# Kernel optimization log

Hardware: AMD Instinct MI355X
Metric: run time of the kernel (lower is better)

## Reference

```python
import jax, jax.numpy as jnp
import numpy as np
from math import sqrt

BASE = 10000.0  # rope_theta
NUM_HEADS = 16


def _quant(x):
    # per-row (last-dim) symmetric int8 fake-quant, matching ActivationQuantSTE.forward
    scale = 127.0 / jnp.maximum(jnp.max(jnp.abs(x), axis=-1, keepdims=True), 1e-5)
    return jnp.clip(jnp.round(x * scale), -128.0, 127.0) / scale


@jax.custom_vjp
def act_quant(x):
    return _quant(x)

def _aq_fwd(x):
    return _quant(x), None

def _aq_bwd(_, g):
    return (g,)  # straight-through estimator

act_quant.defvjp(_aq_fwd, _aq_bwd)


def complex_linear(xr, xi, Wr, Wi):
    # ComplexLinearBase: quantize activations, then
    #   y_real = q_real @ Wr^T + q_imag @ Wi^T
    #   y_imag = q_real @ Wi^T - q_imag @ Wr^T
    qr = act_quant(xr)
    qi = act_quant(xi)
    yr = qr @ Wr.T + qi @ Wi.T
    yi = qr @ Wi.T - qi @ Wr.T
    return yr, yi


def setup_inputs() -> dict:
    T, H = 2048, 2048
    key = jax.random.key(0)
    ks = jax.random.split(key, 10)
    w = lambda k: jax.random.normal(k, (H, H), jnp.float32) * 0.02
    return {
        "hidden_real": jax.random.normal(ks[0], (T, H), jnp.float32),
        "hidden_imag": jax.random.normal(ks[1], (T, H), jnp.float32),
        "positions": jnp.arange(T, dtype=jnp.int32),
        "Wq_r": w(ks[2]), "Wq_i": w(ks[3]),
        "Wk_r": w(ks[4]), "Wk_i": w(ks[5]),
        "Wv_r": w(ks[6]), "Wv_i": w(ks[7]),
        "Wo_r": w(ks[8]), "Wo_i": w(ks[9]),
    }


def reference(hidden_real, hidden_imag, positions, Wq_r, Wq_i, Wk_r, Wk_i, Wv_r, Wv_i, Wo_r, Wo_i):
    T, H = hidden_real.shape
    NH = NUM_HEADS
    D = H // NH  # head_dim

    # complex QKV projections with int8 activation fake-quant
    qr, qi = complex_linear(hidden_real, hidden_imag, Wq_r, Wq_i)
    kr, ki = complex_linear(hidden_real, hidden_imag, Wk_r, Wk_i)
    vr, vi = complex_linear(hidden_real, hidden_imag, Wv_r, Wv_i)

    # Complex RoPE: interleaving (real, imag) then GPT-J-style rotation with
    # head_size = rotary_dim = 2*D is equivalent to rotating (real, imag) pairs:
    #   out_real = real*cos - imag*sin ; out_imag = imag*cos + real*sin
    # inv_freq = base^-(arange(0, 2D, 2)/(2D)) = base^-(arange(D)/D), len D.
    inv_freq = 1.0 / (BASE ** (jnp.arange(D, dtype=jnp.float32) / D))
    freqs = positions.astype(jnp.float32)[:, None] * inv_freq[None, :]  # [T, D]
    # cache is stored in bf16 in the original module
    cos = jnp.cos(freqs).astype(jnp.bfloat16).astype(jnp.float32)[:, None, :]  # [T,1,D]
    sin = jnp.sin(freqs).astype(jnp.bfloat16).astype(jnp.float32)[:, None, :]

    def rope(xr_, xi_):
        r = xr_.reshape(T, NH, D)
        i = xi_.reshape(T, NH, D)
        return r * cos - i * sin, i * cos + r * sin

    qr3, qi3 = rope(qr, qi)
    kr3, ki3 = rope(kr, ki)
    vr3 = vr.reshape(T, NH, D)
    vi3 = vi.reshape(T, NH, D)

    # causal attention; scores = Re(q . conj(k)) / sqrt(2*D)  (complex dim is 2*D)
    scale = 1.0 / sqrt(2 * D)
    scores = (jnp.einsum('thd,shd->hts', qr3, kr3)
              + jnp.einsum('thd,shd->hts', qi3, ki3)) * scale  # [NH, T, T]
    causal = jnp.tril(jnp.ones((T, T), dtype=bool))
    scores = jnp.where(causal[None], scores, -1e9)
    p = jax.nn.softmax(scores, axis=-1)

    out_r = jnp.einsum('hts,shd->thd', p, vr3).reshape(T, H)
    out_i = jnp.einsum('hts,shd->thd', p, vi3).reshape(T, H)

    # complex output projection (with activation fake-quant)
    return complex_linear(out_r, out_i, Wo_r, Wo_i)
```

## Files before the change

### kernel.cpp

```cpp
#include <hip/hip_runtime.h>


typedef float v4f __attribute__((ext_vector_type(4)));
typedef _Float16 v8h __attribute__((ext_vector_type(8)));
typedef _Float16 v4h __attribute__((ext_vector_type(4)));

typedef const __attribute__((address_space(1))) void glob_void;
typedef __attribute__((address_space(3))) void lds_void;

__device__ __forceinline__ void gload16(const _Float16* gp, _Float16* lp) {
  __builtin_amdgcn_global_load_lds((glob_void*)gp, (lds_void*)lp, 16, 0, 0);
}

__device__ __forceinline__ float bf16_rt(float f) {
  union { float f; unsigned u; } a; a.f = f;
  unsigned r = (a.u + 0x7fffu + ((a.u >> 16) & 1u)) & 0xffff0000u;
  union { unsigned u; float f; } b; b.u = r;
  return b.f;
}

#define SBAR()  __builtin_amdgcn_sched_barrier(0)
#define WBAR()  __builtin_amdgcn_s_barrier()
#define LGKM0() asm volatile("s_waitcnt lgkmcnt(0)" ::: "memory")

__global__ __launch_bounds__(512, 2) void gemm_qkv256(
    const _Float16* __restrict__ A, const _Float16* __restrict__ B,
    _Float16* __restrict__ Yq, _Float16* __restrict__ vt)
{
  const int p = blockIdx.x;
  const int xcd = p & 7, s = p >> 3;
  const int mt = s & 7, ntl = s >> 3;
  const int nt = xcd * 8 + ntl;
  const int m0 = mt << 8;
  const int n0 = nt * 192;

  __shared__ __align__(16) _Float16 lds[57344];

  const int tid = threadIdx.x, lane = tid & 63, wave = tid >> 6;
  const int quad = lane >> 4, l15 = lane & 15;
  const int wm = wave >> 2, wn = wave & 3;

  const int rr = tid >> 2;
  const int lc8 = (((tid & 3) ^ ((tid >> 3) & 3)) << 3);
  const _Float16* gA = A + (long long)(m0 + rr) * 4096 + lc8;
  const _Float16* gBj[3];
#pragma unroll
  for (int j = 0; j < 3; ++j) {
    const int ks = (j == 2) || (j == 1 && tid >= 256);
    const int r = j * 128 + (tid >> 2) - ks * 192;
    gBj[j] = B + (long long)(n0 + r) * 4096 + ks * 32 + lc8;
  }

  const int co = ((quad ^ ((l15 >> 1) & 3)) << 3);
  const int aBase = (wm * 128 + l15) * 32 + co;
  const int bBase = (wn * 48 + l15) * 32 + co;

  v4f acc[8][3] = {};

  {
    _Float16* sd = lds + tid * 8;
    gload16(gA, sd);
    gload16(gA + 524288, sd + 4096);
    gload16(gBj[0], sd + 16384);
    gload16(gBj[1], sd + 20480);
    gload16(gA + 32, sd + 8192);
    gload16(gA + 524288 + 32, sd + 12288);
    gload16(gBj[2], sd + 24576);
  }
  asm volatile("s_waitcnt vmcnt(3)" ::: "memory");
  WBAR();

  for (int t = 0; t < 64; ++t) {
    const _Float16* As = lds + (t & 1) * 28672;
    const _Float16* Bs = As + 16384;
    _Float16* sd = lds + ((t & 1) ^ 1) * 28672 + tid * 8;
    const int k1 = (t + 1) << 6;
    const bool stg = (t < 63);

    v8h bf[3], af[4];

    af[0] = *(const v8h*)&As[aBase];
    af[1] = *(const v8h*)&As[aBase + 512];
    af[2] = *(const v8h*)&As[aBase + 1024];
    af[3] = *(const v8h*)&As[aBase + 1536];
    bf[0] = *(const v8h*)&Bs[bBase];
    bf[1] = *(const v8h*)&Bs[bBase + 512];
    bf[2] = *(const v8h*)&Bs[bBase + 1024];
    if (stg) { gload16(gA + k1, sd); gload16(gA + k1 + 524288, sd + 4096); }
    SBAR(); WBAR(); LGKM0(); SBAR();
    __builtin_amdgcn_s_setprio(1);
#pragma unroll
    for (int i = 0; i < 4; ++i)
#pragma unroll
      for (int nf = 0; nf < 3; ++nf)
        acc[i][nf] = __builtin_amdgcn_mfma_f32_16x16x32_f16(af[i], bf[nf], acc[i][nf], 0, 0, 0);
    __builtin_amdgcn_s_setprio(0);
    WBAR();

    af[0] = *(const v8h*)&As[aBase + 2048];
    af[1] = *(const v8h*)&As[aBase + 2560];
    af[2] = *(const v8h*)&As[aBase + 3072];
    af[3] = *(const v8h*)&As[aBase + 3584];
    if (stg) { gload16(gBj[0] + k1, sd + 16384); gload16(gBj[1] + k1, sd + 20480); }
    SBAR(); WBAR(); LGKM0(); SBAR();
    __builtin_amdgcn_s_setprio(1);
#pragma unroll
    for (int i = 0; i < 4; ++i)
#pragma unroll
      for (int nf = 0; nf < 3; ++nf)
        acc[4 + i][nf] = __builtin_amdgcn_mfma_f32_16x16x32_f16(af[i], bf[nf], acc[4 + i][nf], 0, 0, 0);
    __builtin_amdgcn_s_setprio(0);
    if (stg) asm volatile("s_waitcnt vmcnt(4)" ::: "memory");
    else     asm volatile("s_waitcnt vmcnt(0)" ::: "memory");
    WBAR();

    bf[0] = *(const v8h*)&Bs[bBase + 6144];
    bf[1] = *(const v8h*)&Bs[bBase + 6656];
    bf[2] = *(const v8h*)&Bs[bBase + 7168];
    af[0] = *(const v8h*)&As[aBase + 8192];
    af[1] = *(const v8h*)&As[aBase + 8704];
    af[2] = *(const v8h*)&As[aBase + 9216];
    af[3] = *(const v8h*)&As[aBase + 9728];
    if (stg) { gload16(gA + k1 + 32, sd + 8192); gload16(gA + k1 + 524288 + 32, sd + 12288); }
    SBAR(); WBAR(); LGKM0(); SBAR();
    __builtin_amdgcn_s_setprio(1);
#pragma unroll
    for (int i = 0; i < 4; ++i)
#pragma unroll
      for (int nf = 0; nf < 3; ++nf)
        acc[i][nf] = __builtin_amdgcn_mfma_f32_16x16x32_f16(af[i], bf[nf], acc[i][nf], 0, 0, 0);
    __builtin_amdgcn_s_setprio(0);
    WBAR();

    af[0] = *(const v8h*)&As[aBase + 10240];
    af[1] = *(const v8h*)&As[aBase + 10752];
    af[2] = *(const v8h*)&As[aBase + 11264];
    af[3] = *(const v8h*)&As[aBase + 11776];
    if (stg) gload16(gBj[2] + k1, sd + 24576);
    SBAR(); WBAR(); LGKM0(); SBAR();
    __builtin_amdgcn_s_setprio(1);
#pragma unroll
    for (int i = 0; i < 4; ++i)
#pragma unroll
      for (int nf = 0; nf < 3; ++nf)
        acc[4 + i][nf] = __builtin_amdgcn_mfma_f32_16x16x32_f16(af[i], bf[nf], acc[4 + i][nf], 0, 0, 0);
    __builtin_amdgcn_s_setprio(0);
    if (stg) asm volatile("s_waitcnt vmcnt(3)" ::: "memory");
    WBAR();
  }

#pragma unroll
  for (int mf = 0; mf < 8; ++mf) {
#pragma unroll
    for (int nf = 0; nf < 3; ++nf) {
      const int col = n0 + wn * 48 + nf * 16 + l15;
      const int row0 = m0 + wm * 128 + mf * 16 + quad * 4;
      if (col >= 8192) {
        const int c = col - 8192;
        const int hh = (c & 2047) >> 7;
        const int dcol = (c < 2048) ? (c & 127) : (128 + (c & 127));
        v4h pk;
#pragma unroll
        for (int r = 0; r < 4; ++r) pk[r] = (_Float16)acc[mf][nf][r];
        *(v4h*)(vt + ((long long)(hh * 256 + dcol)) * 2048 + row0) = pk;
      } else {
#pragma unroll
        for (int r = 0; r < 4; ++r)
          Yq[(long long)(row0 + r) * 8192 + col] = (_Float16)acc[mf][nf][r];
      }
    }
  }
}

__global__ __launch_bounds__(512, 2) void gemm_out256(
    const _Float16* __restrict__ A, const _Float16* __restrict__ B,
    float* __restrict__ O)
{
  const int p = blockIdx.x;
  const int xcd = p & 7, s = p >> 3;
  const int mt = s & 7, ntl = s >> 3;
  const int nt = xcd * 4 + ntl;
  const int m0 = mt << 8, n0 = nt << 7;

  __shared__ __align__(16) _Float16 lds[49152];

  const int tid = threadIdx.x, lane = tid & 63, wave = tid >> 6;
  const int quad = lane >> 4, l15 = lane & 15;
  const int wm = wave >> 2, wn = wave & 3;

  const int rr = tid >> 2;
  const int lc8 = (((tid & 3) ^ ((tid >> 3) & 3)) << 3);
  const _Float16* gA = A + (long long)(m0 + rr) * 4096 + lc8;
  const _Float16* gB = B + (long long)(n0 + rr) * 4096 + lc8;

  const int co = ((quad ^ ((l15 >> 1) & 3)) << 3);
  const int aBase = (wm * 128 + l15) * 32 + co;
  const int bBase = (wn * 32 + l15) * 32 + co;

  v4f acc[8][2] = {};

  {
    _Float16* sd = lds + tid * 8;
    gload16(gA, sd);
    gload16(gA + 524288, sd + 4096);
    gload16(gB, sd + 16384);
    gload16(gA + 32, sd + 8192);
    gload16(gA + 524288 + 32, sd + 12288);
    gload16(gB + 32, sd + 20480);
  }
  asm volatile("s_waitcnt vmcnt(3)" ::: "memory");
  WBAR();

  for (int t = 0; t < 64; ++t) {
    const _Float16* As = lds + (t & 1) * 24576;
    const _Float16* Bs = As + 16384;
    _Float16* sd = lds + ((t & 1) ^ 1) * 24576 + tid * 8;
    const int k1 = (t + 1) << 6;
    const bool stg = (t < 63);

    v8h bf[2], af[4];

    af[0] = *(const v8h*)&As[aBase];
    af[1] = *(const v8h*)&As[aBase + 512];
    af[2] = *(const v8h*)&As[aBase + 1024];
    af[3] = *(const v8h*)&As[aBase + 1536];
    bf[0] = *(const v8h*)&Bs[bBase];
    bf[1] = *(const v8h*)&Bs[bBase + 512];
    if (stg) { gload16(gA + k1, sd); gload16(gA + k1 + 524288, sd + 4096); }
    SBAR(); WBAR(); LGKM0(); SBAR();
    __builtin_amdgcn_s_setprio(1);
#pragma unroll
    for (int i = 0; i < 4; ++i)
#pragma unroll
      for (int nf = 0; nf < 2; ++nf)
        acc[i][nf] = __builtin_amdgcn_mfma_f32_16x16x32_f16(af[i], bf[nf], acc[i][nf], 0, 0, 0);
    __builtin_amdgcn_s_setprio(0);
    WBAR();

    af[0] = *(const v8h*)&As[aBase + 2048];
    af[1] = *(const v8h*)&As[aBase + 2560];
    af[2] = *(const v8h*)&As[aBase + 3072];
    af[3] = *(const v8h*)&As[aBase + 3584];
    if (stg) gload16(gB + k1, sd + 16384);
    SBAR(); WBAR(); LGKM0(); SBAR();
    __builtin_amdgcn_s_setprio(1);
#pragma unroll
    for (int i = 0; i < 4; ++i)
#pragma unroll
      for (int nf = 0; nf < 2; ++nf)
        acc[4 + i][nf] = __builtin_amdgcn_mfma_f32_16x16x32_f16(af[i], bf[nf], acc[4 + i][nf], 0, 0, 0);
    __builtin_amdgcn_s_setprio(0);
    if (stg) asm volatile("s_waitcnt vmcnt(3)" ::: "memory");
    else     asm volatile("s_waitcnt vmcnt(0)" ::: "memory");
    WBAR();

    bf[0] = *(const v8h*)&Bs[bBase + 4096];
    bf[1] = *(const v8h*)&Bs[bBase + 4608];
    af[0] = *(const v8h*)&As[aBase + 8192];
    af[1] = *(const v8h*)&As[aBase + 8704];
    af[2] = *(const v8h*)&As[aBase + 9216];
    af[3] = *(const v8h*)&As[aBase + 9728];
    if (stg) { gload16(gA + k1 + 32, sd + 8192); gload16(gA + k1 + 524288 + 32, sd + 12288); }
    SBAR(); WBAR(); LGKM0(); SBAR();
    __builtin_amdgcn_s_setprio(1);
#pragma unroll
    for (int i = 0; i < 4; ++i)
#pragma unroll
      for (int nf = 0; nf < 2; ++nf)
        acc[i][nf] = __builtin_amdgcn_mfma_f32_16x16x32_f16(af[i], bf[nf], acc[i][nf], 0, 0, 0);
    __builtin_amdgcn_s_setprio(0);
    WBAR();

    af[0] = *(const v8h*)&As[aBase + 10240];
    af[1] = *(const v8h*)&As[aBase + 10752];
    af[2] = *(const v8h*)&As[aBase + 11264];
    af[3] = *(const v8h*)&As[aBase + 11776];
    if (stg) gload16(gB + k1 + 32, sd + 20480);
    SBAR(); WBAR(); LGKM0(); SBAR();
    __builtin_amdgcn_s_setprio(1);
#pragma unroll
    for (int i = 0; i < 4; ++i)
#pragma unroll
      for (int nf = 0; nf < 2; ++nf)
        acc[4 + i][nf] = __builtin_amdgcn_mfma_f32_16x16x32_f16(af[i], bf[nf], acc[4 + i][nf], 0, 0, 0);
    __builtin_amdgcn_s_setprio(0);
    if (stg) asm volatile("s_waitcnt vmcnt(3)" ::: "memory");
    WBAR();
  }

#pragma unroll
  for (int mf = 0; mf < 8; ++mf) {
#pragma unroll
    for (int nf = 0; nf < 2; ++nf) {
      const int col = n0 + wn * 32 + nf * 16 + l15;
      const int row0 = m0 + wm * 128 + mf * 16 + quad * 4;
#pragma unroll
      for (int r = 0; r < 4; ++r) {
        const int row = row0 + r;
        const float v = acc[mf][nf][r];
        if (col < 2048) O[(long long)row * 2048 + col] = v;
        else O[2048ll * 2048 + (long long)row * 2048 + (col - 2048)] = v;
      }
    }
  }
}

__global__ __launch_bounds__(256) void quant_rows(
    const float* __restrict__ s0, const float* __restrict__ s1,
    _Float16* __restrict__ dst)
{
  const int t = blockIdx.x, y = blockIdx.y;
  const float* src = (y ? s1 : s0) + (long long)t * 2048;
  const int tid = threadIdx.x, lane = tid & 63, wave = tid >> 6;
  __shared__ float rbuf[4];
  const v4f a = *(const v4f*)(src + tid * 4);
  const v4f b = *(const v4f*)(src + 1024 + tid * 4);
  float m = 0.f;
#pragma unroll
  for (int k = 0; k < 4; ++k)
    m = fmaxf(m, fmaxf(fabsf(a[k]), fabsf(b[k])));
  for (int o = 1; o < 64; o <<= 1) m = fmaxf(m, __shfl_xor(m, o, 64));
  if (lane == 0) rbuf[wave] = m;
  __syncthreads();
  m = fmaxf(fmaxf(rbuf[0], rbuf[1]), fmaxf(rbuf[2], rbuf[3]));
  const float scale = 127.f / fmaxf(m, 1e-5f);
  const float inv = 1.f / scale;
  _Float16* d = dst + (long long)t * 4096 + (long long)y * 2048 + tid * 4;
  v4h qa, qb;
#pragma unroll
  for (int k = 0; k < 4; ++k) {
    qa[k] = (_Float16)(fminf(fmaxf(rintf(a[k] * scale), -128.f), 127.f) * inv);
    qb[k] = (_Float16)(fminf(fmaxf(rintf(b[k] * scale), -128.f), 127.f) * inv);
  }
  *(v4h*)d = qa;
  *(v4h*)(d + 1024) = qb;
}

__global__ __launch_bounds__(256) void wprep(
    const float* __restrict__ Wq_r, const float* __restrict__ Wq_i,
    const float* __restrict__ Wk_r, const float* __restrict__ Wk_i,
    const float* __restrict__ Wv_r, const float* __restrict__ Wv_i,
    const float* __restrict__ Wo_r, const float* __restrict__ Wo_i,
    _Float16* __restrict__ Bqkv, _Float16* __restrict__ Bo)
{
  const float* Ws[8] = {Wq_r, Wq_i, Wk_r, Wk_i, Wv_r, Wv_i, Wo_r, Wo_i};
  const int i = blockIdx.x * 256 + threadIdx.x;
  const int w = i >> 18;
  const int rem = i & 262143;
  const int j = rem >> 7;
  const int cb = (rem & 127) * 16;
  const float* src = Ws[w] + (long long)j * 2048 + cb;
  _Float16* Bp = (w < 6) ? (Bqkv + (long long)(w >> 1) * 4096 * 4096) : Bo;
  const int isI = w & 1;
  _Float16* d1 = Bp + (long long)j * 4096 + (isI ? 2048 + cb : cb);
  _Float16* d2 = Bp + (long long)(2048 + j) * 4096 + (isI ? cb : 2048 + cb);
  const float sg2 = isI ? 1.f : -1.f;
#pragma unroll
  for (int q = 0; q < 4; ++q) {
    const v4f v = *(const v4f*)(src + q * 4);
    v4h o1, o2;
#pragma unroll
    for (int k = 0; k < 4; ++k) {
      o1[k] = (_Float16)v[k];
      o2[k] = (_Float16)(v[k] * sg2);
    }
    *(v4h*)(d1 + q * 4) = o1;
    *(v4h*)(d2 + q * 4) = o2;
  }
}

__global__ __launch_bounds__(256) void trig_kernel(
    const int* __restrict__ pos, float* __restrict__ cs)
{
  const int t = blockIdx.x * 2 + (threadIdx.x >> 7);
  const int d = threadIdx.x & 127;
  const float invf = (float)pow(10000.0, -(double)d / 128.0);
  const float fr = (float)pos[t] * invf;
  const double fd = (double)fr;
  cs[((long long)t * 128 + d) * 2]     = bf16_rt((float)cos(fd));
  cs[((long long)t * 128 + d) * 2 + 1] = bf16_rt((float)sin(fd));
}

__global__ __launch_bounds__(256) void rope_kernel(
    const _Float16* __restrict__ Yq, const float* __restrict__ cs,
    _Float16* __restrict__ qc, _Float16* __restrict__ kc)
{
  const int idx = blockIdx.x * 256 + threadIdx.x;
  const int d0 = (idx & 15) * 8;
  const int h  = (idx >> 4) & 15;
  const int t  = idx >> 8;
  const _Float16* y = Yq + (long long)t * 8192 + h * 128 + d0;
  const v8h qr8 = *(const v8h*)(y);
  const v8h qi8 = *(const v8h*)(y + 2048);
  const v8h kr8 = *(const v8h*)(y + 4096);
  const v8h ki8 = *(const v8h*)(y + 6144);
  const float* cp = cs + ((long long)t * 128 + d0) * 2;
  v8h qro, qio, kro, kio;
#pragma unroll
  for (int u = 0; u < 8; ++u) {
    const float c = cp[u * 2], s = cp[u * 2 + 1];
    const float qr = (float)qr8[u], qi = (float)qi8[u];
    const float kr = (float)kr8[u], ki = (float)ki8[u];
    qro[u] = (_Float16)(qr * c - qi * s);
    qio[u] = (_Float16)(qi * c + qr * s);
    kro[u] = (_Float16)(kr * c - ki * s);
    kio[u] = (_Float16)(ki * c + kr * s);
  }
  _Float16* qo = qc + ((long long)h * 2048 + t) * 256 + d0;
  _Float16* ko = kc + ((long long)h * 2048 + t) * 256 + d0;
  *(v8h*)qo = qro; *(v8h*)(qo + 128) = qio;
  *(v8h*)ko = kro; *(v8h*)(ko + 128) = kio;
}

__global__ __launch_bounds__(256, 2) void flash_attn(
    const _Float16* __restrict__ qc, const _Float16* __restrict__ kc,
    const _Float16* __restrict__ vt, float* __restrict__ attn)
{
  __shared__ __align__(16) _Float16 Ps[64 * 136];
  __shared__ float pmax[2][64];
  __shared__ float psum[2][64];

  const int h  = blockIdx.y;
  const int qt = ((h >> 3) & 1) ? (31 - (int)blockIdx.x) : (int)blockIdx.x;
  const int q0 = qt * 64;
  const int tid = threadIdx.x, lane = tid & 63, wave = tid >> 6;
  const int mi = wave >> 1, ni = wave & 1;
  const int quad = lane >> 4, l15 = lane & 15;

  const _Float16* qh = qc + (long long)h * 2048 * 256;
  const _Float16* kh = kc + (long long)h * 2048 * 256;
  const _Float16* vh = vt + (long long)h * 256 * 2048;

  const _Float16 scl = (_Float16)0.09016844f;
  v8h qf[2][8];
#pragma unroll
  for (int mt = 0; mt < 2; ++mt) {
    const int t = q0 + mi * 32 + mt * 16 + l15;
#pragma unroll
    for (int ks = 0; ks < 8; ++ks) {
      v8h q = *(const v8h*)(qh + (long long)t * 256 + ks * 32 + quad * 8);
#pragma unroll
      for (int u = 0; u < 8; ++u) q[u] *= scl;
      qf[mt][ks] = q;
    }
  }

  float mrow[2][4], lrow[2][4];
  v4f acc_o[2][8];
#pragma unroll
  for (int mt = 0; mt < 2; ++mt)
#pragma unroll
    for (int r = 0; r < 4; ++r) { mrow[mt][r] = -1e30f; lrow[mt][r] = 0.f; }
#pragma unroll
  for (int mt = 0; mt < 2; ++mt)
#pragma unroll
    for (int nt = 0; nt < 8; ++nt) acc_o[mt][nt] = (v4f){0.f, 0.f, 0.f, 0.f};

  const int nst = (qt >> 1) + 1;
  for (int st = 0; st < nst; ++st) {
    const int s0 = st * 128;
    const bool diag = (st == nst - 1);

    bool live[4];
#pragma unroll
    for (int jn = 0; jn < 4; ++jn)
      live[jn] = !diag || (s0 + ni * 64 + jn * 16 <= q0 + 63);

    v4f sa[2][4] = {};
#pragma unroll
    for (int ks = 0; ks < 8; ++ks) {
      v8h bk[4];
#pragma unroll
      for (int jn = 0; jn < 4; ++jn)
        if (live[jn])
          bk[jn] = *(const v8h*)(kh + (long long)(s0 + ni * 64 + jn * 16 + l15) * 256
                                 + ks * 32 + quad * 8);
#pragma unroll
      for (int mt = 0; mt < 2; ++mt)
#pragma unroll
        for (int jn = 0; jn < 4; ++jn)
          if (live[jn])
            sa[mt][jn] = __builtin_amdgcn_mfma_f32_16x16x32_f16(qf[mt][ks], bk[jn], sa[mt][jn], 0, 0, 0);
    }

    float pm[2][4];
#pragma unroll
    for (int mt = 0; mt < 2; ++mt)
#pragma unroll
      for (int r = 0; r < 4; ++r) pm[mt][r] = -1e30f;
#pragma unroll
    for (int mt = 0; mt < 2; ++mt)
#pragma unroll
      for (int jn = 0; jn < 4; ++jn)
#pragma unroll
        for (int r = 0; r < 4; ++r) {
          float v = sa[mt][jn][r];
          if (diag) {
            const int rl = q0 + mi * 32 + mt * 16 + quad * 4 + r;
            const int cl = s0 + ni * 64 + jn * 16 + l15;
            if (cl > rl) v = -1e30f;
          }
          sa[mt][jn][r] = v;
          pm[mt][r] = fmaxf(pm[mt][r], v);
        }
#pragma unroll
    for (int o = 1; o < 16; o <<= 1)
#pragma unroll
      for (int mt = 0; mt < 2; ++mt)
#pragma unroll
        for (int r = 0; r < 4; ++r)
          pm[mt][r] = fmaxf(pm[mt][r], __shfl_xor(pm[mt][r], o, 64));
    if (l15 == 0) {
#pragma unroll
      for (int mt = 0; mt < 2; ++mt)
#pragma unroll
        for (int r = 0; r < 4; ++r)
          pmax[ni][mi * 32 + mt * 16 + quad * 4 + r] = pm[mt][r];
    }
    __syncthreads();

    float al[2][4], ps[2][4];
#pragma unroll
    for (int mt = 0; mt < 2; ++mt)
#pragma unroll
      for (int r = 0; r < 4; ++r) {
        const int row = mi * 32 + mt * 16 + quad * 4 + r;
        const float mn = fmaxf(mrow[mt][r], fmaxf(pmax[0][row], pmax[1][row]));
        al[mt][r] = __builtin_amdgcn_exp2f(mrow[mt][r] - mn);
        mrow[mt][r] = mn;
        ps[mt][r] = 0.f;
      }
#pragma unroll
    for (int mt = 0; mt < 2; ++mt)
#pragma unroll
      for (int jn = 0; jn < 4; ++jn)
#pragma unroll
        for (int r = 0; r < 4; ++r) {
          const float e = __builtin_amdgcn_exp2f(sa[mt][jn][r] - mrow[mt][r]);
          ps[mt][r] += e;
          Ps[(mi * 32 + mt * 16 + quad * 4 + r) * 136 + ni * 64 + jn * 16 + l15] = (_Float16)e;
        }
#pragma unroll
    for (int o = 1; o < 16; o <<= 1)
#pragma unroll
      for (int mt = 0; mt < 2; ++mt)
#pragma unroll
        for (int r = 0; r < 4; ++r)
          ps[mt][r] += __shfl_xor(ps[mt][r], o, 64);
    if (l15 == 0) {
#pragma unroll
      for (int mt = 0; mt < 2; ++mt)
#pragma unroll
        for (int r = 0; r < 4; ++r)
          psum[ni][mi * 32 + mt * 16 + quad * 4 + r] = ps[mt][r];
    }
    __syncthreads();

#pragma unroll
    for (int mt = 0; mt < 2; ++mt)
#pragma unroll
      for (int r = 0; r < 4; ++r) {
        const int row = mi * 32 + mt * 16 + quad * 4 + r;
        lrow[mt][r] = lrow[mt][r] * al[mt][r] + psum[0][row] + psum[1][row];
      }
#pragma unroll
    for (int mt = 0; mt < 2; ++mt)
#pragma unroll
      for (int nt = 0; nt < 8; ++nt)
#pragma unroll
        for (int r = 0; r < 4; ++r)
          acc_o[mt][nt][r] *= al[mt][r];

#pragma unroll
    for (int kc2 = 0; kc2 < 4; ++kc2) {
      if (diag && (s0 + kc2 * 32 > q0 + 63)) continue;
      v8h pa[2];
#pragma unroll
      for (int mt = 0; mt < 2; ++mt) {
        const int row = mi * 32 + mt * 16 + l15;
        pa[mt] = *(const v8h*)(Ps + row * 136 + kc2 * 32 + quad * 8);
      }
#pragma unroll
      for (int nt = 0; nt < 8; ++nt) {
        const v8h vb = *(const v8h*)(vh + (long long)(ni * 128 + nt * 16 + l15) * 2048
                                     + s0 + kc2 * 32 + quad * 8);
#pragma unroll
        for (int mt = 0; mt < 2; ++mt)
          acc_o[mt][nt] = __builtin_amdgcn_mfma_f32_16x16x32_f16(pa[mt], vb, acc_o[mt][nt], 0, 0, 0);
      }
    }
  }

#pragma unroll
  for (int mt = 0; mt < 2; ++mt) {
    float inv[4];
#pragma unroll
    for (int r = 0; r < 4; ++r) inv[r] = 1.f / lrow[mt][r];
#pragma unroll
    for (int nt = 0; nt < 8; ++nt) {
      const int d = ni * 128 + nt * 16 + l15;
      float* dst = attn + ((d < 128) ? 0ll : (2048ll * 2048)) + (h * 128 + (d & 127));
#pragma unroll
      for (int r = 0; r < 4; ++r) {
        const int t = q0 + mi * 32 + mt * 16 + quad * 4 + r;
        dst[(long long)t * 2048] = acc_o[mt][nt][r] * inv[r];
      }
    }
  }
}

extern "C" void kernel_launch(void* const* d_in, const int* in_sizes, int n_in,
                              void* d_out, int out_size, void* d_ws, size_t ws_size,
                              hipStream_t stream) {
  const float* hr   = (const float*)d_in[0];
  const float* hi   = (const float*)d_in[1];
  const int*   pos  = (const int*)d_in[2];
  const float* Wq_r = (const float*)d_in[3];
  const float* Wq_i = (const float*)d_in[4];
  const float* Wk_r = (const float*)d_in[5];
  const float* Wk_i = (const float*)d_in[6];
  const float* Wv_r = (const float*)d_in[7];
  const float* Wv_i = (const float*)d_in[8];
  const float* Wo_r = (const float*)d_in[9];
  const float* Wo_i = (const float*)d_in[10];

  char* ws = (char*)d_ws;
  _Float16* Bqkv = (_Float16*)(ws);
  float*    attn = (float*)   (ws);
  float*    cs   = (float*)   (ws + (32ll  << 20));
  _Float16* Bo   = (_Float16*)(ws + (96ll  << 20));
  _Float16* Ac   = (_Float16*)(ws + (128ll << 20));
  _Float16* Yq   = (_Float16*)(ws + (144ll << 20));
  _Float16* qc   = (_Float16*)(ws + (176ll << 20));
  _Float16* kc   = (_Float16*)(ws + (192ll << 20));
  _Float16* vt   = (_Float16*)(ws + (208ll << 20));

  quant_rows<<<dim3(2048, 2), 256, 0, stream>>>(hr, hi, Ac);
  wprep<<<8192, 256, 0, stream>>>(Wq_r, Wq_i, Wk_r, Wk_i, Wv_r, Wv_i, Wo_r, Wo_i, Bqkv, Bo);
  gemm_qkv256<<<512, 512, 0, stream>>>(Ac, Bqkv, Yq, vt);
  trig_kernel<<<1024, 256, 0, stream>>>(pos, cs);
  rope_kernel<<<2048, 256, 0, stream>>>(Yq, cs, qc, kc);
  flash_attn<<<dim3(32, 16), 256, 0, stream>>>(qc, kc, vt, attn);
  quant_rows<<<dim3(2048, 2), 256, 0, stream>>>(attn, attn + 2048ll * 2048, Ac);
  gemm_out256<<<256, 512, 0, stream>>>(Ac, Bo, (float*)d_out);
}
```

Before: 686.0 us.

## Split causal flash attention KV range across two blocks and add combine kernel

Flash attention gets a third grid dimension of 2. Each block handles every other 128-key stage and writes its unnormalized partial output plus per-row max and sum. A new fa_combine kernel merges the two partials with log-sum-exp weights and writes the normalized result in the layout the next stage expects. The goal is to double the number of blocks and even out the causal triangle's uneven work per block, at the cost of an extra 64 MB of partial-output writes and reads and one more launch.

Result: slower. 709.6 us (+3.4%).

```diff
diff --git a/kernel.cpp b/kernel.cpp
--- a/kernel.cpp
+++ b/kernel.cpp
@@ -414,13 +414,15 @@
 
 __global__ __launch_bounds__(256, 2) void flash_attn(
     const _Float16* __restrict__ qc, const _Float16* __restrict__ kc,
-    const _Float16* __restrict__ vt, float* __restrict__ attn)
+    const _Float16* __restrict__ vt, float* __restrict__ opart,
+    float* __restrict__ ml)
 {
   __shared__ __align__(16) _Float16 Ps[64 * 136];
   __shared__ float pmax[2][64];
   __shared__ float psum[2][64];
 
   const int h  = blockIdx.y;
+  const int z  = blockIdx.z;
   const int qt = ((h >> 3) & 1) ? (31 - (int)blockIdx.x) : (int)blockIdx.x;
   const int q0 = qt * 64;
   const int tid = threadIdx.x, lane = tid & 63, wave = tid >> 6;
@@ -457,7 +459,7 @@
     for (int nt = 0; nt < 8; ++nt) acc_o[mt][nt] = (v4f){0.f, 0.f, 0.f, 0.f};
 
   const int nst = (qt >> 1) + 1;
-  for (int st = 0; st < nst; ++st) {
+  for (int st = z; st < nst; st += 2) {
     const int s0 = st * 128;
     const bool diag = (st == nst - 1);
 
@@ -591,22 +593,52 @@
     }
   }
 
-#pragma unroll
-  for (int mt = 0; mt < 2; ++mt) {
-    float inv[4];
-#pragma unroll
-    for (int r = 0; r < 4; ++r) inv[r] = 1.f / lrow[mt][r];
+  float* Od = opart + (long long)(z * 16 + h) * 2048 * 256;
+  if (ni == 0 && l15 == 0) {
+    float2* mlp = (float2*)ml + (long long)(z * 16 + h) * 2048;
+#pragma unroll
+    for (int mt = 0; mt < 2; ++mt)
+#pragma unroll
+      for (int r = 0; r < 4; ++r) {
+        const int t = q0 + mi * 32 + mt * 16 + quad * 4 + r;
+        mlp[t] = make_float2(mrow[mt][r], lrow[mt][r]);
+      }
+  }
+#pragma unroll
+  for (int mt = 0; mt < 2; ++mt)
 #pragma unroll
     for (int nt = 0; nt < 8; ++nt) {
       const int d = ni * 128 + nt * 16 + l15;
-      float* dst = attn + ((d < 128) ? 0ll : (2048ll * 2048)) + (h * 128 + (d & 127));
 #pragma unroll
       for (int r = 0; r < 4; ++r) {
         const int t = q0 + mi * 32 + mt * 16 + quad * 4 + r;
-        dst[(long long)t * 2048] = acc_o[mt][nt][r] * inv[r];
-      }
-    }
-  }
+        Od[(long long)t * 256 + d] = acc_o[mt][nt][r];
+      }
+    }
+}
+
+__global__ __launch_bounds__(256) void fa_combine(
+    const float* __restrict__ opart, const float* __restrict__ ml,
+    float* __restrict__ attn)
+{
+  const int idx = blockIdx.x * 256 + threadIdx.x;
+  const int d4 = (idx & 63) * 4;
+  const int t  = (idx >> 6) & 2047;
+  const int h  = idx >> 17;
+  const float2 a = ((const float2*)ml)[h * 2048 + t];
+  const float2 b = ((const float2*)ml)[(16 + h) * 2048 + t];
+  const float ms = fmaxf(a.x, b.x);
+  const float w0 = __builtin_amdgcn_exp2f(a.x - ms);
+  const float w1 = __builtin_amdgcn_exp2f(b.x - ms);
+  const float inv = 1.f / (a.y * w0 + b.y * w1);
+  const v4f o0 = *(const v4f*)(opart + ((long long)h * 2048 + t) * 256 + d4);
+  const v4f o1 = *(const v4f*)(opart + ((long long)(16 + h) * 2048 + t) * 256 + d4);
+  v4f o;
+#pragma unroll
+  for (int k = 0; k < 4; ++k) o[k] = (o0[k] * w0 + o1[k] * w1) * inv;
+  float* dst = attn + ((d4 < 128) ? 0ll : (2048ll * 2048))
+             + (long long)t * 2048 + h * 128 + (d4 & 127);
+  *(v4f*)dst = o;
 }
 
 extern "C" void kernel_launch(void* const* d_in, const int* in_sizes, int n_in,
@@ -625,22 +657,25 @@
   const float* Wo_i = (const float*)d_in[10];
 
   char* ws = (char*)d_ws;
-  _Float16* Bqkv = (_Float16*)(ws);
-  float*    attn = (float*)   (ws);
-  float*    cs   = (float*)   (ws + (32ll  << 20));
-  _Float16* Bo   = (_Float16*)(ws + (96ll  << 20));
-  _Float16* Ac   = (_Float16*)(ws + (128ll << 20));
-  _Float16* Yq   = (_Float16*)(ws + (144ll << 20));
-  _Float16* qc   = (_Float16*)(ws + (176ll << 20));
-  _Float16* kc   = (_Float16*)(ws + (192ll << 20));
-  _Float16* vt   = (_Float16*)(ws + (208ll << 20));
+  _Float16* Bqkv  = (_Float16*)(ws);
+  float*    attn  = (float*)   (ws);
+  float*    cs    = (float*)   (ws + (32ll  << 20));
+  float*    opart = (float*)   (ws + (32ll  << 20));
+  _Float16* Bo    = (_Float16*)(ws + (96ll  << 20));
+  _Float16* Ac    = (_Float16*)(ws + (128ll << 20));
+  _Float16* Yq    = (_Float16*)(ws + (144ll << 20));
+  float*    mlbuf = (float*)   (ws + (144ll << 20));
+  _Float16* qc    = (_Float16*)(ws + (176ll << 20));
+  _Float16* kc    = (_Float16*)(ws + (192ll << 20));
+  _Float16* vt    = (_Float16*)(ws + (208ll << 20));
 
   quant_rows<<<dim3(2048, 2), 256, 0, stream>>>(hr, hi, Ac);
   wprep<<<8192, 256, 0, stream>>>(Wq_r, Wq_i, Wk_r, Wk_i, Wv_r, Wv_i, Wo_r, Wo_i, Bqkv, Bo);
   gemm_qkv256<<<512, 512, 0, stream>>>(Ac, Bqkv, Yq, vt);
   trig_kernel<<<1024, 256, 0, stream>>>(pos, cs);
   rope_kernel<<<2048, 256, 0, stream>>>(Yq, cs, qc, kc);
-  flash_attn<<<dim3(32, 16), 256, 0, stream>>>(qc, kc, vt, attn);
+  flash_attn<<<dim3(32, 16, 2), 256, 0, stream>>>(qc, kc, vt, opart, mlbuf);
+  fa_combine<<<8192, 256, 0, stream>>>(opart, mlbuf, attn);
   quant_rows<<<dim3(2048, 2), 256, 0, stream>>>(attn, attn + 2048ll * 2048, Ac);
   gemm_out256<<<256, 512, 0, stream>>>(Ac, Bo, (float*)d_out);
 }
```
